# Optimization experiments

Hardware: AMD Instinct MI355X
Metric: run time of the kernel (lower is better)

## Reference

```python
import jax, jax.numpy as jnp
import numpy as np

W = 8            # fine window (sqrt of feat_0's WW)
WP2 = W + 2      # feat_1 search window side (10)
SLICE = 8
TEMP = 10.0


def setup_inputs() -> dict:
    key = jax.random.key(0)
    ks = jax.random.split(key, 6)
    M = 8192
    C = 64
    return {
        'feat_0': jax.random.normal(ks[0], (M, W * W, C), dtype=jnp.float32),
        'feat_1': jax.random.normal(ks[1], (M, WP2 * WP2, C), dtype=jnp.float32),
        'mkpts0_c': jax.random.uniform(ks[2], (M, 2), dtype=jnp.float32) * 800.0,
        'mkpts1_c': jax.random.uniform(ks[3], (M, 2), dtype=jnp.float32) * 800.0,
        'mconf': jax.random.uniform(ks[4], (M,), dtype=jnp.float32),
        'b_ids': jnp.zeros((M,), dtype=jnp.int64),
        'hw0_i': 832,
        'hw0_f': 416,
        'bs': 1,
    }


def reference(feat_0, feat_1, mkpts0_c, mkpts1_c, mconf, b_ids, hw0_i, hw0_f, bs):
    M, WW, C = feat_0.shape                      # WW = W*W = 64
    scale = float(hw0_i) / float(hw0_f)          # image -> fine-feature stride

    feat_f0, feat_ff0 = feat_0[..., :-SLICE], feat_0[..., -SLICE:]
    feat_f1, feat_ff1 = feat_1[..., :-SLICE], feat_1[..., -SLICE:]

    # note: BOTH sides divided by sqrt(C) in the source -> overall 1/C
    conf_f = jnp.einsum('mlc,mrc->mlr', feat_f0, feat_f1) * (1.0 / C)          # [M,64,100]
    conf_ff = jnp.einsum('mlc,mrc->mlr', feat_ff0, feat_ff1) / np.sqrt(SLICE)  # [M,64,100]

    # dual softmax, then crop the 10x10 search window to the inner 8x8
    sm = jax.nn.softmax(conf_f, axis=1) * jax.nn.softmax(conf_f, axis=2)
    sm = sm.reshape(M, WW, WP2, WP2)[..., 1:-1, 1:-1].reshape(M, WW, WW)       # [M,64,64]

    # ---- get_fine_ds_match (torch.no_grad in source) ----
    flat = jax.lax.stop_gradient(sm.reshape(M, WW * WW))
    idx = jnp.argmax(flat, axis=-1)                # [M]
    idx_l, idx_r = idx // WW, idx % WW             # each in [0,64)
    gy, gx = jnp.meshgrid(jnp.arange(W), jnp.arange(W), indexing='ij')
    grid = (jnp.stack([gx, gy], -1).reshape(WW, 2).astype(feat_0.dtype)
            - (W // 2) + 0.5)                      # (x,y) pixel offsets, centered
    delta_l = grid[idx_l]                          # [M,2]
    delta_r = grid[idx_r]
    mkpts0_f = jax.lax.stop_gradient(mkpts0_c) + delta_l * scale
    mkpts1_mid = jax.lax.stop_gradient(mkpts1_c) + delta_r * scale

    # ---- 3x3 window gather in the (W+2)x(W+2) map (faithful index arithmetic) ----
    iids, jids = idx_r // W, idx_r % W             # [0,8)
    d = jnp.arange(3) - 1                          # {-1,0,1}
    wi = iids[:, None, None] + d[None, :, None]    # [M,3,3] rows, may be -1
    wj = jids[:, None, None] + d[None, None, :]    # [M,3,3] cols
    wi = jnp.where(wi < 0, wi + WP2, wi)           # torch negative-index wrap
    wj = jnp.where(wj < 0, wj + WP2, wj)
    cff = conf_ff.reshape(M, WW, WP2, WP2)
    win = cff[jnp.arange(M)[:, None, None], idx_l[:, None, None], wi, wj]  # [M,3,3]

    probs = jax.nn.softmax(win.reshape(M, 9) / TEMP, axis=-1)              # [M,9]
    heat = probs.reshape(M, 3, 3)
    pos = jnp.linspace(-1.0, 1.0, 3).astype(feat_0.dtype)
    coord_x = jnp.sum(heat * pos[None, None, :], axis=(1, 2))              # over width
    coord_y = jnp.sum(heat * pos[None, :, None], axis=(1, 2))              # over height
    coords = jnp.stack([coord_x, coord_y], -1)     # [M,2] soft-argmax, (x,y)

    scale1 = scale                                 # bs == 1 branch
    mkpts1_f = mkpts1_mid + coords * (3 // 2) * scale1
    return (mkpts0_f, mkpts1_f, probs, sm)
```

## Files before the change

kernel.cpp:

```cpp
#include <hip/hip_runtime.h>
#include <math.h>
#include <limits.h>


constexpr int TPB = 256;

typedef _Float16 half8_t __attribute__((ext_vector_type(8)));
typedef _Float16 half4_t __attribute__((ext_vector_type(4)));
typedef float    float4_t __attribute__((ext_vector_type(4)));

struct __align__(16) SMem {
    union {
        struct {
            unsigned short f1h[100 * 56];
            unsigned short f1l[100 * 56];
        };
        struct {
            float sm[64 * 64];
            float cpart[4][112];
            float csum[112];
            float wval[4];
            int   widx[4];
            float win[9];
        };
    };
};

__global__ __launch_bounds__(TPB, 7) void fine_matching_kernel(
    const float* __restrict__ feat0,
    const float* __restrict__ feat1,
    const float* __restrict__ mk0,
    const float* __restrict__ mk1,
    const int* __restrict__ hw0_i,
    const int* __restrict__ hw0_f,
    float* __restrict__ out, int M)
{
    __shared__ SMem S;

    const int m = blockIdx.x;
    const int t = threadIdx.x;
    const int lane = t & 63;
    const int w = t >> 6;
    const int col = lane & 15;
    const int q = lane >> 4;
    const float scale = (float)hw0_i[0] / (float)hw0_f[0];

    const float* g0 = feat0 + (size_t)m * 4096;
    const float* g1 = feat1 + (size_t)m * 6400;
    _Float16* f1h = (_Float16*)S.f1h;
    _Float16* f1l = (_Float16*)S.f1l;

    const int arow = (16 * w + col) * 64;
    float4_t araw[2][2];
    #pragma unroll
    for (int ks = 0; ks < 2; ks++) {
        const int koff = ks ? (32 + q * 8) : (q * 8);
        araw[ks][0] = *(const float4_t*)(g0 + arow + koff);
        araw[ks][1] = *(const float4_t*)(g0 + arow + koff + 4);
    }

    for (int i = t; i < 700; i += TPB) {
        const int l = i / 7;
        const int c = (i - l * 7) * 8;
        const float* src = g1 + l * 64 + c;
        float4_t v0 = *(const float4_t*)(src);
        float4_t v1 = *(const float4_t*)(src + 4);
        half8_t hi, lo;
        #pragma unroll
        for (int k = 0; k < 4; k++) {
            float x = v0[k];
            _Float16 h = (_Float16)x;
            hi[k] = h;
            lo[k] = (_Float16)(x - (float)h);
        }
        #pragma unroll
        for (int k = 0; k < 4; k++) {
            float x = v1[k];
            _Float16 h = (_Float16)x;
            hi[4 + k] = h;
            lo[4 + k] = (_Float16)(x - (float)h);
        }
        *(half8_t*)(f1h + l * 56 + c) = hi;
        *(half8_t*)(f1l + l * 56 + c) = lo;
    }

    half8_t hz;
    #pragma unroll
    for (int j = 0; j < 8; j++) hz[j] = (_Float16)0.0f;

    half8_t ah[2], al[2];
    #pragma unroll
    for (int ks = 0; ks < 2; ks++) {
        #pragma unroll
        for (int j = 0; j < 8; j++) {
            float x = araw[ks][j >> 2][j & 3];
            _Float16 h = (_Float16)x;
            ah[ks][j] = h;
            al[ks][j] = (_Float16)(x - (float)h);
        }
    }
    if (q == 3) { ah[1] = hz; al[1] = hz; }

    __syncthreads();

    float4_t acc[7];
    #pragma unroll
    for (int rt = 0; rt < 7; rt++)
        #pragma unroll
        for (int j = 0; j < 4; j++) acc[rt][j] = 0.0f;

    #pragma unroll
    for (int ks = 0; ks < 2; ks++) {
        const int koff = ks ? (32 + q * 8) : (q * 8);
        const bool kz = (ks == 1) && (q == 3);
        const int bkoff = kz ? 0 : koff;
        #pragma unroll
        for (int rt = 0; rt < 7; rt++) {
            int brow = rt * 16 + col;
            if (brow > 99) brow = 99;
            const int bo = brow * 56 + bkoff;
            half8_t bh = *(const half8_t*)(f1h + bo);
            half8_t bl = *(const half8_t*)(f1l + bo);
            acc[rt] = __builtin_amdgcn_mfma_f32_16x16x32_f16(ah[ks], bh, acc[rt], 0, 0, 0);
            acc[rt] = __builtin_amdgcn_mfma_f32_16x16x32_f16(al[ks], bh, acc[rt], 0, 0, 0);
            acc[rt] = __builtin_amdgcn_mfma_f32_16x16x32_f16(ah[ks], bl, acc[rt], 0, 0, 0);
        }
    }

    __syncthreads();

    float p[7][4];
    #pragma unroll
    for (int rt = 0; rt < 7; rt++) {
        const bool rvalid = (rt < 6) || (col < 4);
        #pragma unroll
        for (int j = 0; j < 4; j++) {
            float c = acc[rt][j] * (1.0f / 64.0f);
            p[rt][j] = rvalid ? __expf(c) : 0.0f;
        }
    }

    float invr[4];
    #pragma unroll
    for (int j = 0; j < 4; j++) {
        float s = 0.0f;
        #pragma unroll
        for (int rt = 0; rt < 7; rt++) s += p[rt][j];
        s += __shfl_xor(s, 1); s += __shfl_xor(s, 2);
        s += __shfl_xor(s, 4); s += __shfl_xor(s, 8);
        invr[j] = 1.0f / s;
    }

    #pragma unroll
    for (int rt = 0; rt < 7; rt++) {
        float s = p[rt][0] + p[rt][1] + p[rt][2] + p[rt][3];
        s += __shfl_xor(s, 16);
        s += __shfl_xor(s, 32);
        if (lane < 16) S.cpart[w][rt * 16 + col] = s;
    }
    __syncthreads();
    if (t < 112)
        S.csum[t] = S.cpart[0][t] + S.cpart[1][t] + S.cpart[2][t] + S.cpart[3][t];
    __syncthreads();

    float invc[7];
    #pragma unroll
    for (int rt = 0; rt < 7; rt++) {
        const bool rvalid = (rt < 6) || (col < 4);
        invc[rt] = rvalid ? 1.0f / S.csum[rt * 16 + col] : 0.0f;
    }

    float* s_sm = S.sm;
    float bestv = -INFINITY; int besti = INT_MAX;
    #pragma unroll
    for (int j = 0; j < 4; j++) {
        const int l = 16 * w + 4 * q + j;
        #pragma unroll
        for (int rt = 0; rt < 7; rt++) {
            const int r = rt * 16 + col;
            if (r < 100) {
                const int ri = r / 10, rj = r - ri * 10;
                if (ri >= 1 && ri <= 8 && rj >= 1 && rj <= 8) {
                    float pv = p[rt][j];
                    float v = pv * pv * invr[j] * invc[rt];
                    int flat = l * 64 + (ri - 1) * 8 + (rj - 1);
                    s_sm[flat] = v;
                    if (v > bestv) { bestv = v; besti = flat; }
                }
            }
        }
    }
    #pragma unroll
    for (int d = 1; d < 64; d <<= 1) {
        float ov = __shfl_xor(bestv, d);
        int   oi = __shfl_xor(besti, d);
        if (ov > bestv || (ov == bestv && oi < besti)) { bestv = ov; besti = oi; }
    }
    if (lane == 0) { S.wval[w] = bestv; S.widx[w] = besti; }
    __syncthreads();

    float bv = S.wval[0]; int best = S.widx[0];
    #pragma unroll
    for (int i = 1; i < 4; i++) {
        float v2 = S.wval[i]; int i2 = S.widx[i];
        if (v2 > bv || (v2 == bv && i2 < best)) { bv = v2; best = i2; }
    }
    const int idx_l = best >> 6;
    const int idx_r = best & 63;
    const int iids  = idx_r >> 3, jids = idx_r & 7;

    float* o_sm = out + (size_t)13 * M + (size_t)m * 4096;
    for (int i = t; i < 1024; i += TPB)
        ((float4_t*)o_sm)[i] = ((const float4_t*)s_sm)[i];

    if (t < 9) {
        int da = t / 3 - 1, db = t % 3 - 1;
        int wi = iids + da; if (wi < 0) wi += 10;
        int wj = jids + db; if (wj < 0) wj += 10;
        int rp = wi * 10 + wj;
        float4_t a0 = *(const float4_t*)(g0 + idx_l * 64 + 56);
        float4_t a1 = *(const float4_t*)(g0 + idx_l * 64 + 60);
        float4_t b0 = *(const float4_t*)(g1 + rp * 64 + 56);
        float4_t b1 = *(const float4_t*)(g1 + rp * 64 + 60);
        float dot = 0.0f;
        #pragma unroll
        for (int j = 0; j < 4; j++) dot += a0[j] * b0[j] + a1[j] * b1[j];
        S.win[t] = dot * 0.35355339059327373f;
    }
    __syncthreads();

    if (t == 0) {
        float ww[9], mx = -INFINITY;
        #pragma unroll
        for (int i = 0; i < 9; i++) { ww[i] = S.win[i] * 0.1f; mx = fmaxf(mx, ww[i]); }
        float sum = 0.0f;
        #pragma unroll
        for (int i = 0; i < 9; i++) { ww[i] = __expf(ww[i] - mx); sum += ww[i]; }
        float inv = 1.0f / sum;
        float* o_probs = out + (size_t)4 * M + (size_t)m * 9;
        float cx = 0.0f, cy = 0.0f;
        #pragma unroll
        for (int i = 0; i < 9; i++) {
            float pb = ww[i] * inv;
            o_probs[i] = pb;
            cx += pb * (float)(i % 3 - 1);
            cy += pb * (float)(i / 3 - 1);
        }
        float dlx = (float)(idx_l & 7) - 3.5f;
        float dly = (float)(idx_l >> 3) - 3.5f;
        out[2 * m]     = mk0[2 * m]     + dlx * scale;
        out[2 * m + 1] = mk0[2 * m + 1] + dly * scale;
        float drx = (float)jids - 3.5f;
        float dry = (float)iids - 3.5f;
        float* o1 = out + (size_t)2 * M;
        o1[2 * m]     = mk1[2 * m]     + (drx + cx) * scale;
        o1[2 * m + 1] = mk1[2 * m + 1] + (dry + cy) * scale;
    }
}

extern "C" void kernel_launch(void* const* d_in, const int* in_sizes, int n_in,
                              void* d_out, int out_size, void* d_ws, size_t ws_size,
                              hipStream_t stream) {
    const float* feat0 = (const float*)d_in[0];
    const float* feat1 = (const float*)d_in[1];
    const float* mk0   = (const float*)d_in[2];
    const float* mk1   = (const float*)d_in[3];
    const int*   hw0_i = (const int*)d_in[6];
    const int*   hw0_f = (const int*)d_in[7];
    const int M = in_sizes[0] / 4096;

    fine_matching_kernel<<<M, TPB, 0, stream>>>(
        feat0, feat1, mk0, mk1, hw0_i, hw0_f, (float*)d_out, M);
}
```

Before: 418.8 us.

## Write sm output directly from registers, prefetch feat1 loads, use fast exp2/rcp

Drops the 16KB shared-memory staging buffer for the softmax product and has each thread store its sm values straight to global memory at the end of the kernel. The feat1 tile loads are issued up front, unrolled into three fixed chunks, so more loads are in flight before the fp16 split. Exp and reciprocal are replaced with hardware exp2/rcp builtins, and the mkpts reads are moved early. The direct global stores are scattered scalar writes instead of coalesced float4 stores, which may cost write efficiency, while the smaller LDS footprint could allow more resident blocks.

```diff
diff --git a/kernel.cpp b/kernel.cpp
--- a/kernel.cpp
+++ b/kernel.cpp
@@ -6,8 +6,8 @@
 constexpr int TPB = 256;
 
 typedef _Float16 half8_t __attribute__((ext_vector_type(8)));
-typedef _Float16 half4_t __attribute__((ext_vector_type(4)));
 typedef float    float4_t __attribute__((ext_vector_type(4)));
+typedef float    float2_t __attribute__((ext_vector_type(2)));
 
 struct __align__(16) SMem {
     union {
@@ -16,7 +16,6 @@
             unsigned short f1l[100 * 56];
         };
         struct {
-            float sm[64 * 64];
             float cpart[4][112];
             float csum[112];
             float wval[4];
@@ -25,6 +24,36 @@
         };
     };
 };
+
+__device__ __forceinline__ float fast_rcp(float x) {
+#if __has_builtin(__builtin_amdgcn_rcpf)
+    return __builtin_amdgcn_rcpf(x);
+#else
+    return 1.0f / x;
+#endif
+}
+
+__device__ __forceinline__ float fast_exp2(float x) {
+#if __has_builtin(__builtin_amdgcn_exp2f)
+    return __builtin_amdgcn_exp2f(x);
+#else
+    return __expf(x * 0.69314718055994530942f);
+#endif
+}
+
+__device__ __forceinline__ void split8(float4_t a, float4_t b,
+                                       half8_t& hi, half8_t& lo) {
+    #pragma unroll
+    for (int k = 0; k < 4; k++) {
+        float x = a[k]; _Float16 h = (_Float16)x;
+        hi[k] = h; lo[k] = (_Float16)(x - (float)h);
+    }
+    #pragma unroll
+    for (int k = 0; k < 4; k++) {
+        float x = b[k]; _Float16 h = (_Float16)x;
+        hi[4 + k] = h; lo[4 + k] = (_Float16)(x - (float)h);
+    }
+}
 
 __global__ __launch_bounds__(TPB, 7) void fine_matching_kernel(
     const float* __restrict__ feat0,
@@ -50,6 +79,22 @@
     _Float16* f1h = (_Float16*)S.f1h;
     _Float16* f1l = (_Float16*)S.f1l;
 
+    const float2_t mkv0 = *(const float2_t*)(mk0 + 2 * m);
+    const float2_t mkv1 = *(const float2_t*)(mk1 + 2 * m);
+
+    const int c0 = t, c1 = t + 256;
+    const bool h2 = (t < 188);
+    const int c2 = h2 ? (t + 512) : t;
+    const int l0g = c0 / 7, k0 = (c0 - l0g * 7) * 8;
+    const int l1g = c1 / 7, k1 = (c1 - l1g * 7) * 8;
+    const int l2g = c2 / 7, k2 = (c2 - l2g * 7) * 8;
+    float4_t u0a = *(const float4_t*)(g1 + l0g * 64 + k0);
+    float4_t u0b = *(const float4_t*)(g1 + l0g * 64 + k0 + 4);
+    float4_t u1a = *(const float4_t*)(g1 + l1g * 64 + k1);
+    float4_t u1b = *(const float4_t*)(g1 + l1g * 64 + k1 + 4);
+    float4_t u2a = *(const float4_t*)(g1 + l2g * 64 + k2);
+    float4_t u2b = *(const float4_t*)(g1 + l2g * 64 + k2 + 4);
+
     const int arow = (16 * w + col) * 64;
     float4_t araw[2][2];
     #pragma unroll
@@ -59,29 +104,20 @@
         araw[ks][1] = *(const float4_t*)(g0 + arow + koff + 4);
     }
 
-    for (int i = t; i < 700; i += TPB) {
-        const int l = i / 7;
-        const int c = (i - l * 7) * 8;
-        const float* src = g1 + l * 64 + c;
-        float4_t v0 = *(const float4_t*)(src);
-        float4_t v1 = *(const float4_t*)(src + 4);
-        half8_t hi, lo;
-        #pragma unroll
-        for (int k = 0; k < 4; k++) {
-            float x = v0[k];
-            _Float16 h = (_Float16)x;
-            hi[k] = h;
-            lo[k] = (_Float16)(x - (float)h);
-        }
-        #pragma unroll
-        for (int k = 0; k < 4; k++) {
-            float x = v1[k];
-            _Float16 h = (_Float16)x;
-            hi[4 + k] = h;
-            lo[4 + k] = (_Float16)(x - (float)h);
-        }
-        *(half8_t*)(f1h + l * 56 + c) = hi;
-        *(half8_t*)(f1l + l * 56 + c) = lo;
+    {
+        half8_t hi, lo; split8(u0a, u0b, hi, lo);
+        *(half8_t*)(f1h + l0g * 56 + k0) = hi;
+        *(half8_t*)(f1l + l0g * 56 + k0) = lo;
+    }
+    {
+        half8_t hi, lo; split8(u1a, u1b, hi, lo);
+        *(half8_t*)(f1h + l1g * 56 + k1) = hi;
+        *(half8_t*)(f1l + l1g * 56 + k1) = lo;
+    }
+    if (h2) {
+        half8_t hi, lo; split8(u2a, u2b, hi, lo);
+        *(half8_t*)(f1h + l2g * 56 + k2) = hi;
+        *(half8_t*)(f1l + l2g * 56 + k2) = lo;
     }
 
     half8_t hz;
@@ -129,15 +165,14 @@
 
     __syncthreads();
 
+    constexpr float CC = 1.44269504088896340736f / 64.0f;
     float p[7][4];
     #pragma unroll
     for (int rt = 0; rt < 7; rt++) {
         const bool rvalid = (rt < 6) || (col < 4);
         #pragma unroll
-        for (int j = 0; j < 4; j++) {
-            float c = acc[rt][j] * (1.0f / 64.0f);
-            p[rt][j] = rvalid ? __expf(c) : 0.0f;
-        }
+        for (int j = 0; j < 4; j++)
+            p[rt][j] = rvalid ? fast_exp2(acc[rt][j] * CC) : 0.0f;
     }
 
     float invr[4];
@@ -148,7 +183,7 @@
         for (int rt = 0; rt < 7; rt++) s += p[rt][j];
         s += __shfl_xor(s, 1); s += __shfl_xor(s, 2);
         s += __shfl_xor(s, 4); s += __shfl_xor(s, 8);
-        invr[j] = 1.0f / s;
+        invr[j] = fast_rcp(s);
     }
 
     #pragma unroll
@@ -167,10 +202,10 @@
     #pragma unroll
     for (int rt = 0; rt < 7; rt++) {
         const bool rvalid = (rt < 6) || (col < 4);
-        invc[rt] = rvalid ? 1.0f / S.csum[rt * 16 + col] : 0.0f;
-    }
-
-    float* s_sm = S.sm;
+        invc[rt] = rvalid ? fast_rcp(S.csum[rt * 16 + col]) : 0.0f;
+    }
+
+    float v[7][4];
     float bestv = -INFINITY; int besti = INT_MAX;
     #pragma unroll
     for (int j = 0; j < 4; j++) {
@@ -178,14 +213,14 @@
         #pragma unroll
         for (int rt = 0; rt < 7; rt++) {
             const int r = rt * 16 + col;
-            if (r < 100) {
+            if ((rt < 6) || (col < 4)) {
                 const int ri = r / 10, rj = r - ri * 10;
                 if (ri >= 1 && ri <= 8 && rj >= 1 && rj <= 8) {
                     float pv = p[rt][j];
-                    float v = pv * pv * invr[j] * invc[rt];
+                    float val = pv * pv * invr[j] * invc[rt];
+                    v[rt][j] = val;
                     int flat = l * 64 + (ri - 1) * 8 + (rj - 1);
-                    s_sm[flat] = v;
-                    if (v > bestv) { bestv = v; besti = flat; }
+                    if (val > bestv) { bestv = val; besti = flat; }
                 }
             }
         }
@@ -208,10 +243,6 @@
     const int idx_l = best >> 6;
     const int idx_r = best & 63;
     const int iids  = idx_r >> 3, jids = idx_r & 7;
-
-    float* o_sm = out + (size_t)13 * M + (size_t)m * 4096;
-    for (int i = t; i < 1024; i += TPB)
-        ((float4_t*)o_sm)[i] = ((const float4_t*)s_sm)[i];
 
     if (t < 9) {
         int da = t / 3 - 1, db = t % 3 - 1;
@@ -248,13 +279,29 @@
         }
         float dlx = (float)(idx_l & 7) - 3.5f;
         float dly = (float)(idx_l >> 3) - 3.5f;
-        out[2 * m]     = mk0[2 * m]     + dlx * scale;
-        out[2 * m + 1] = mk0[2 * m + 1] + dly * scale;
+        out[2 * m]     = mkv0[0] + dlx * scale;
+        out[2 * m + 1] = mkv0[1] + dly * scale;
         float drx = (float)jids - 3.5f;
         float dry = (float)iids - 3.5f;
         float* o1 = out + (size_t)2 * M;
-        o1[2 * m]     = mk1[2 * m]     + (drx + cx) * scale;
-        o1[2 * m + 1] = mk1[2 * m + 1] + (dry + cy) * scale;
+        o1[2 * m]     = mkv1[0] + (drx + cx) * scale;
+        o1[2 * m + 1] = mkv1[1] + (dry + cy) * scale;
+    }
+
+    float* o_sm = out + (size_t)13 * M + (size_t)m * 4096;
+    const int lbase = (16 * w + 4 * q) * 64;
+    #pragma unroll
+    for (int rt = 0; rt < 7; rt++) {
+        const int r = rt * 16 + col;
+        if ((rt < 6) || (col < 4)) {
+            const int ri = r / 10, rj = r - ri * 10;
+            if (ri >= 1 && ri <= 8 && rj >= 1 && rj <= 8) {
+                const int base = lbase + (ri - 1) * 8 + (rj - 1);
+                #pragma unroll
+                for (int j = 0; j < 4; j++)
+                    o_sm[base + j * 64] = v[rt][j];
+            }
+        }
     }
 }
 
```

Measured after the change: 415.5 us. No clear change (-0.8%).
